# Performance work log

Hardware: AMD Instinct MI355X
Metric: run time of the kernel (lower is better)

Reference implementation:

```python
import jax, jax.numpy as jnp
import numpy as np

KERNEL = 4  # conv kernel == stride (non-overlapping patches)


def _conv(x, W, b):
    # x: [B, Cin, H, W], W: [Cout, Cin, k, k] (OIHW), stride == kernel, VALID padding
    y = jax.lax.conv_general_dilated(
        x, W, window_strides=(KERNEL, KERNEL), padding='VALID',
        dimension_numbers=('NCHW', 'OIHW', 'NCHW'))
    return y + b[None, :, None, None]


def setup_inputs() -> dict:
    key = jax.random.key(0)
    ks = jax.random.split(key, 7)
    B, Cin, H, Wd = 4, 64, 256, 256
    Cout = 128
    s = 0.05
    return {
        'x': jax.random.normal(ks[0], (B, Cin, H, Wd), dtype=jnp.float32),
        'Wq': jax.random.normal(ks[1], (Cout, Cin, KERNEL, KERNEL), dtype=jnp.float32) * s,
        'bq': jax.random.normal(ks[2], (Cout,), dtype=jnp.float32) * s,
        'Wk': jax.random.normal(ks[3], (Cout, Cin, KERNEL, KERNEL), dtype=jnp.float32) * s,
        'bk': jax.random.normal(ks[4], (Cout,), dtype=jnp.float32) * s,
        'Wv': jax.random.normal(ks[5], (Cout, Cin, KERNEL, KERNEL), dtype=jnp.float32) * s,
        'bv': jax.random.normal(ks[6], (Cout,), dtype=jnp.float32) * s,
    }


def reference(x, Wq, bq, Wk, bk, Wv, bv):
    B = x.shape[0]
    q = _conv(x, Wq, bq)              # [B, O, Hp, Wp]
    O, Hp, Wp = q.shape[1], q.shape[2], q.shape[3]
    N = Hp * Wp
    q = q.reshape(B, O, N)
    k = _conv(x, Wk, bk).reshape(B, O, N)
    v = _conv(x, Wv, bv).reshape(B, O, N)
    # scores[b, n, m] = sum_o q[b,o,n] * k[b,o,m]  (NO scaling, as in original)
    scores = jnp.einsum('bon,bom->bnm', q, k)
    attn = jax.nn.softmax(scores, axis=-1)        # [B, N, N]
    # attended^T: out[b, o, n] = sum_m attn[b,n,m] * v[b,o,m]
    out = jnp.einsum('bnm,bom->bon', attn, v)
    return out.reshape(B, O, Hp, Wp)
```

## Files before the change

### kernel.cpp

```cpp
#include <hip/hip_runtime.h>
#include <cstdint>
#include <cstddef>

#define NB 4
#define NP 4096
#define OD 128

typedef _Float16 h16;
typedef _Float16 h16x8 __attribute__((ext_vector_type(8)));
typedef _Float16 h16x4 __attribute__((ext_vector_type(4)));
typedef float    f32x4 __attribute__((ext_vector_type(4)));

__device__ __forceinline__ void async16(const void* g, void* l) {
    __builtin_amdgcn_global_load_lds(
        (const __attribute__((address_space(1))) void*)g,
        (__attribute__((address_space(3))) void*)l, 16, 0, 0);
}

__global__ __launch_bounds__(256) void wcvt(
    const float* __restrict__ Wq, const float* __restrict__ Wk,
    const float* __restrict__ Wv, h16* __restrict__ W16s)
{
    int g = blockIdx.x * 256 + threadIdx.x;
    int mat = g >> 14, r = g & 16383;
    int kc = r >> 9, q = r & 511, o = q >> 2, csw = q & 3;
    int c = csw ^ ((o >> 1) & 3);
    const float* W = (mat == 0) ? Wq : (mat == 1) ? Wk : Wv;
    const float* src = W + (size_t)o * 1024 + kc * 32 + 8 * c;
    f32x4 a = *(const f32x4*)src;
    f32x4 b = *(const f32x4*)(src + 4);
    h16x8 h = {(h16)a.x, (h16)a.y, (h16)a.z, (h16)a.w,
               (h16)b.x, (h16)b.y, (h16)b.z, (h16)b.w};
    *(h16x8*)&W16s[(size_t)g * 8] = h;
}

__global__ __launch_bounds__(256, 2) void conv_qkv(
    const float* __restrict__ x, const h16* __restrict__ W16s,
    const float* __restrict__ bq, const float* __restrict__ bk,
    const float* __restrict__ bv,
    h16* __restrict__ qt, h16* __restrict__ kt, h16* __restrict__ vt)
{
    const int nt = blockIdx.x;
    const int b  = blockIdx.y;
    const int tid = threadIdx.x, lane = tid & 63, wv = tid >> 6;
    const int lr = lane & 15, qd = lane >> 4;
    const int o_w = 32 * wv;

    __shared__ __align__(16) char smem[85504];
    float* biasl = (float*)(smem + 83968);
    if (tid < 128) {
        biasl[tid] = bq[tid]; biasl[128 + tid] = bk[tid]; biasl[256 + tid] = bv[tid];
    }

    auto dmaW = [&](int kc, int bs) {
#pragma unroll
        for (int t = 0; t < 6; ++t) {
            int grp = wv * 6 + t;
            int mat = grp >> 3, sg = grp & 7;
            async16(W16s + ((size_t)(mat * 32 + kc) * 512 + sg * 64 + lane) * 8,
                    smem + bs * 24576 + mat * 8192 + sg * 1024);
        }
    };

    f32x4 xr[2][2];
    auto xload = [&](int kc, int sl) {
        int n = tid >> 2, kg = tid & 3;
        int c = kg >> 1, kh2 = (kg & 1) * 2;
        const float* p = &x[(((size_t)(b * 64 + 2 * kc + c) * 256) + 4 * nt + kh2) * 256 + 4 * n];
        xr[sl][0] = *(const f32x4*)p;
        xr[sl][1] = *(const f32x4*)(p + 256);
    };
    auto xwrite = [&](int sl, int xbs) {
        int n = tid >> 2, kg = tid & 3;
        int c = kg >> 1, kh2 = (kg & 1) * 2;
        h16x8 h = {(h16)xr[sl][0].x, (h16)xr[sl][0].y, (h16)xr[sl][0].z, (h16)xr[sl][0].w,
                   (h16)xr[sl][1].x, (h16)xr[sl][1].y, (h16)xr[sl][1].z, (h16)xr[sl][1].w};
        *(h16x8*)(smem + 73728 + xbs * 5120 + n * 80 + c * 32 + kh2 * 8) = h;
    };

    f32x4 acc[3][2][4];
#pragma unroll
    for (int m = 0; m < 3; ++m)
#pragma unroll
        for (int a = 0; a < 2; ++a)
#pragma unroll
            for (int c = 0; c < 4; ++c) acc[m][a][c] = (f32x4){0.f, 0.f, 0.f, 0.f};

    xload(0, 0); dmaW(0, 0);
    xload(1, 1); dmaW(1, 1);
    xwrite(0, 0);
    __syncthreads();

    int wb = 0;
#pragma unroll 2
    for (int kc = 0; kc < 32; ++kc) {
        int xbs = kc & 1;
        if (kc + 2 < 32) {
            dmaW(kc + 2, (wb == 0) ? 2 : wb - 1);
            xload(kc + 2, xbs);
        }
        const h16* Xl = (const h16*)(smem + 73728 + xbs * 5120);
        const char* Wl = smem + wb * 24576;

        h16x8 bf[4];
#pragma unroll
        for (int tn = 0; tn < 4; ++tn)
            bf[tn] = *(const h16x8*)&Xl[(16 * tn + lr) * 40 + 8 * qd];
#pragma unroll
        for (int mat = 0; mat < 3; ++mat) {
            h16x8 af[2];
#pragma unroll
            for (int to = 0; to < 2; ++to) {
                int o = o_w + 16 * to + lr;
                af[to] = *(const h16x8*)(Wl + mat * 8192 + (size_t)(o * 4 + (qd ^ ((o >> 1) & 3))) * 16);
            }
#pragma unroll
            for (int to = 0; to < 2; ++to)
#pragma unroll
                for (int tn = 0; tn < 4; ++tn)
                    acc[mat][to][tn] = __builtin_amdgcn_mfma_f32_16x16x32_f16(af[to], bf[tn], acc[mat][to][tn], 0, 0, 0);
        }
        if (kc + 1 < 32) xwrite((kc + 1) & 1, 1 - xbs);
        wb = (wb == 2) ? 0 : wb + 1;
        __syncthreads();
    }

    const int n0 = nt * 64;
#pragma unroll
    for (int mat = 0; mat < 2; ++mat) {
        h16* bnc = (h16*)smem;
#pragma unroll
        for (int to = 0; to < 2; ++to)
#pragma unroll
            for (int tn = 0; tn < 4; ++tn) {
                int ob = o_w + 16 * to + 4 * qd;
                int n  = 16 * tn + lr;
                h16x4 hv = {(h16)(acc[mat][to][tn][0] + biasl[mat * 128 + ob]),
                            (h16)(acc[mat][to][tn][1] + biasl[mat * 128 + ob + 1]),
                            (h16)(acc[mat][to][tn][2] + biasl[mat * 128 + ob + 2]),
                            (h16)(acc[mat][to][tn][3] + biasl[mat * 128 + ob + 3])};
                *(h16x4*)&bnc[n * 136 + ob] = hv;
            }
        __syncthreads();
        h16* dst = mat ? kt : qt;
#pragma unroll
        for (int j = 0; j < 4; ++j) {
            int s = tid + 256 * j;
            int n = s >> 4, oc = s & 15;
            *(h16x8*)(dst + ((size_t)(b * NP + n0 + n)) * OD + 8 * oc) = *(h16x8*)&bnc[n * 136 + 8 * oc];
        }
        __syncthreads();
    }
    {
        h16* bnc = (h16*)smem;
#pragma unroll
        for (int to = 0; to < 2; ++to)
#pragma unroll
            for (int tn = 0; tn < 4; ++tn)
#pragma unroll
                for (int r = 0; r < 4; ++r) {
                    int o = o_w + 16 * to + 4 * qd + r;
                    int n = 16 * tn + lr;
                    bnc[o * 72 + n] = (h16)(acc[2][to][tn][r] + biasl[256 + o]);
                }
        __syncthreads();
#pragma unroll
        for (int j = 0; j < 4; ++j) {
            int s = tid + 256 * j;
            int o = s >> 3, ch = s & 7;
            int g = ch >> 2, q2 = ch & 3;
            h16x8 hv;
#pragma unroll
            for (int r2 = 0; r2 < 8; ++r2) {
                int mt = r2 >> 2, r = r2 & 3;
                hv[r2] = bnc[o * 72 + 32 * g + 16 * mt + 4 * q2 + r];
            }
            *(h16x8*)(vt + ((size_t)(b * OD + o)) * NP + n0 + 32 * g + 8 * q2) = hv;
        }
    }
}

template <int SP>
__global__ __launch_bounds__(256, 3) void flash_attn(
    const h16* __restrict__ qt, const h16* __restrict__ kt,
    const h16* __restrict__ vt, h16* __restrict__ po, float2* __restrict__ ml)
{
    constexpr int MR  = NP / SP;
    constexpr int NIT = MR / 32;
    const int nt = blockIdx.x, sp = blockIdx.y, b = blockIdx.z;
    const int tid = threadIdx.x, lane = tid & 63, wv = tid >> 6;
    const int lr = lane & 15, qd = lane >> 4;

    __shared__ __align__(16) char smem[32768];

    h16x8 qf[2][4];
#pragma unroll
    for (int rt = 0; rt < 2; ++rt)
#pragma unroll
        for (int kc = 0; kc < 4; ++kc)
            qf[rt][kc] = *(const h16x8*)&qt[((size_t)(b * NP + nt * 128 + 32 * wv + 16 * rt + lr)) * OD
                                            + 32 * kc + 8 * qd];

    float m_run[2] = {-1e30f, -1e30f}, l_run[2] = {0.f, 0.f};
    f32x4 oacc[2][8];
#pragma unroll
    for (int rt = 0; rt < 2; ++rt)
#pragma unroll
        for (int t = 0; t < 8; ++t) oacc[rt][t] = (f32x4){0.f, 0.f, 0.f, 0.f};

    auto dma = [&](int it, int bs) {
        int m0 = sp * MR + it * 32;
#pragma unroll
        for (int t = 0; t < 2; ++t) {
            int s = wv * 128 + t * 64 + lane;
            int m = s >> 4, cst = s & 15, csrc = cst ^ (m & 15);
            async16(kt + ((size_t)(b * NP + m0 + m)) * OD + 8 * csrc,
                    smem + bs * 8192 + (wv * 128 + t * 64) * 16);
        }
#pragma unroll
        for (int t = 0; t < 2; ++t) {
            int s = wv * 128 + t * 64 + lane;
            int o = s >> 2, cst = s & 3, csrc = cst ^ ((o >> 1) & 3);
            async16(vt + ((size_t)(b * OD + o)) * NP + m0 + 8 * csrc,
                    smem + 16384 + bs * 8192 + (wv * 128 + t * 64) * 16);
        }
    };

    dma(0, 0);
    __syncthreads();

#pragma unroll 2
    for (int it = 0; it < NIT; ++it) {
        int c = it & 1;
        if (it + 1 < NIT) dma(it + 1, 1 - c);
        const h16* Kb = (const h16*)(smem + c * 8192);
        const h16* Vb = (const h16*)(smem + 16384 + c * 8192);

        f32x4 sc[2][2];
#pragma unroll
        for (int rt = 0; rt < 2; ++rt)
#pragma unroll
            for (int mt = 0; mt < 2; ++mt) sc[rt][mt] = (f32x4){0.f, 0.f, 0.f, 0.f};
#pragma unroll
        for (int mt = 0; mt < 2; ++mt)
#pragma unroll
            for (int kc = 0; kc < 4; ++kc) {
                h16x8 kf = *(const h16x8*)&Kb[(size_t)((16 * mt + lr) * 16 + ((4 * kc + qd) ^ lr)) * 8];
                sc[0][mt] = __builtin_amdgcn_mfma_f32_16x16x32_f16(kf, qf[0][kc], sc[0][mt], 0, 0, 0);
                sc[1][mt] = __builtin_amdgcn_mfma_f32_16x16x32_f16(kf, qf[1][kc], sc[1][mt], 0, 0, 0);
            }

        h16x4 pf[2][2];
        float al[2];
#pragma unroll
        for (int rt = 0; rt < 2; ++rt) {
            float mx = fmaxf(fmaxf(fmaxf(sc[rt][0][0], sc[rt][0][1]), fmaxf(sc[rt][0][2], sc[rt][0][3])),
                             fmaxf(fmaxf(sc[rt][1][0], sc[rt][1][1]), fmaxf(sc[rt][1][2], sc[rt][1][3])));
            mx = fmaxf(mx, __shfl_xor(mx, 16));
            mx = fmaxf(mx, __shfl_xor(mx, 32));
            float mn = fmaxf(m_run[rt], mx);
            al[rt] = __expf(m_run[rt] - mn);
            m_run[rt] = mn;
            float rs = 0.f;
#pragma unroll
            for (int mt = 0; mt < 2; ++mt)
#pragma unroll
                for (int r = 0; r < 4; ++r) {
                    float e = __expf(sc[rt][mt][r] - mn);
                    sc[rt][mt][r] = e;
                    rs += e;
                }
            rs += __shfl_xor(rs, 16);
            rs += __shfl_xor(rs, 32);
            l_run[rt] = l_run[rt] * al[rt] + rs;
            pf[rt][0] = (h16x4){(h16)sc[rt][0][0], (h16)sc[rt][0][1], (h16)sc[rt][0][2], (h16)sc[rt][0][3]};
            pf[rt][1] = (h16x4){(h16)sc[rt][1][0], (h16)sc[rt][1][1], (h16)sc[rt][1][2], (h16)sc[rt][1][3]};
        }
#pragma unroll
        for (int rt = 0; rt < 2; ++rt)
#pragma unroll
            for (int to = 0; to < 8; ++to)
#pragma unroll
                for (int r = 0; r < 4; ++r) oacc[rt][to][r] *= al[rt];

#pragma unroll
        for (int to = 0; to < 8; ++to) {
            int o = 16 * to + lr;
            h16x8 vv = *(const h16x8*)&Vb[(size_t)(o * 4 + (qd ^ ((o >> 1) & 3))) * 8];
            h16x4 va = __builtin_shufflevector(vv, vv, 0, 1, 2, 3);
            h16x4 vb2 = __builtin_shufflevector(vv, vv, 4, 5, 6, 7);
#pragma unroll
            for (int rt = 0; rt < 2; ++rt) {
                oacc[rt][to] = __builtin_amdgcn_mfma_f32_16x16x16f16(va,  pf[rt][0], oacc[rt][to], 0, 0, 0);
                oacc[rt][to] = __builtin_amdgcn_mfma_f32_16x16x16f16(vb2, pf[rt][1], oacc[rt][to], 0, 0, 0);
            }
        }
        __syncthreads();
    }

    const size_t nbase = (size_t)(sp * NB + b) * NP + nt * 128 + 32 * wv;
    if (qd == 0) {
#pragma unroll
        for (int rt = 0; rt < 2; ++rt)
            ml[nbase + 16 * rt + lr] = make_float2(m_run[rt], l_run[rt]);
    }
    float inv[2] = {1.f / l_run[0], 1.f / l_run[1]};
#pragma unroll
    for (int rt = 0; rt < 2; ++rt)
#pragma unroll
        for (int to = 0; to < 8; ++to) {
            h16x4 hv = {(h16)(oacc[rt][to][0] * inv[rt]), (h16)(oacc[rt][to][1] * inv[rt]),
                        (h16)(oacc[rt][to][2] * inv[rt]), (h16)(oacc[rt][to][3] * inv[rt])};
            *(h16x4*)&po[(nbase + 16 * rt + lr) * OD + 16 * to + 4 * qd] = hv;
        }
}

template <int SP>
__global__ __launch_bounds__(256) void combine(
    const h16* __restrict__ po, const float2* __restrict__ ml,
    float* __restrict__ out)
{
    const int nt = blockIdx.x, b = blockIdx.y;
    const int n0 = nt * 64, tid = threadIdx.x;
    __shared__ float w[SP][64];
    __shared__ float bn[64 * 130];

    if (tid < 64) {
        int n = n0 + tid;
        float m[SP], l[SP], M = -1e30f;
#pragma unroll
        for (int s = 0; s < SP; ++s) {
            float2 v = ml[(size_t)(s * NB + b) * NP + n];
            m[s] = v.x; l[s] = v.y;
            M = fmaxf(M, m[s]);
        }
        float d = 0.f, e[SP];
#pragma unroll
        for (int s = 0; s < SP; ++s) { e[s] = l[s] * __expf(m[s] - M); d += e[s]; }
        float id = 1.f / d;
#pragma unroll
        for (int s = 0; s < SP; ++s) w[s][tid] = e[s] * id;
    }
    __syncthreads();

#pragma unroll
    for (int j = 0; j < 4; ++j) {
        int s = tid + 256 * j;
        int n = s >> 4, oc = s & 15;
        float acc[8];
#pragma unroll
        for (int k = 0; k < 8; ++k) acc[k] = 0.f;
#pragma unroll
        for (int sp = 0; sp < SP; ++sp) {
            h16x8 v = *(const h16x8*)&po[((size_t)(sp * NB + b) * NP + n0 + n) * OD + 8 * oc];
            float ww = w[sp][n];
#pragma unroll
            for (int k = 0; k < 8; ++k) acc[k] += ww * (float)v[k];
        }
#pragma unroll
        for (int k = 0; k < 8; ++k) bn[n * 130 + 8 * oc + k] = acc[k];
    }
    __syncthreads();

#pragma unroll
    for (int j = 0; j < 8; ++j) {
        int s = tid + 256 * j;
        int o = s >> 4, n4 = s & 15;
        f32x4 r = {bn[(4 * n4 + 0) * 130 + o], bn[(4 * n4 + 1) * 130 + o],
                   bn[(4 * n4 + 2) * 130 + o], bn[(4 * n4 + 3) * 130 + o]};
        *(f32x4*)&out[((size_t)(b * OD + o)) * NP + n0 + 4 * n4] = r;
    }
}

extern "C" void kernel_launch(void* const* d_in, const int* in_sizes, int n_in,
                              void* d_out, int out_size, void* d_ws, size_t ws_size,
                              hipStream_t stream) {
    const float* x  = (const float*)d_in[0];
    const float* Wq = (const float*)d_in[1];
    const float* bq = (const float*)d_in[2];
    const float* Wk = (const float*)d_in[3];
    const float* bk = (const float*)d_in[4];
    const float* Wv = (const float*)d_in[5];
    const float* bv = (const float*)d_in[6];

    h16* qtp  = (h16*)d_ws;
    h16* ktp  = qtp + (size_t)NB * NP * OD;
    h16* vtp  = ktp + (size_t)NB * NP * OD;
    h16* W16s = vtp + (size_t)NB * NP * OD;
    h16* po   = W16s + (size_t)3 * 32 * 512 * 8;
    float* out = (float*)d_out;

    wcvt<<<dim3(192), 256, 0, stream>>>(Wq, Wk, Wv, W16s);
    conv_qkv<<<dim3(64, NB), 256, 0, stream>>>(x, W16s, bq, bk, bv, qtp, ktp, vtp);

    const size_t base = 13369344;
    const size_t need8 = base + (size_t)8 * NB * NP * OD * 2 + (size_t)8 * NB * NP * 8;
    if (ws_size >= need8) {
        float2* ml = (float2*)(po + (size_t)8 * NB * NP * OD);
        flash_attn<8><<<dim3(32, 8, NB), 256, 0, stream>>>(qtp, ktp, vtp, po, ml);
        combine<8><<<dim3(64, NB), 256, 0, stream>>>(po, ml, out);
    } else {
        float2* ml = (float2*)(po + (size_t)4 * NB * NP * OD);
        flash_attn<4><<<dim3(32, 4, NB), 256, 0, stream>>>(qtp, ktp, vtp, po, ml);
        combine<4><<<dim3(64, NB), 256, 0, stream>>>(po, ml, out);
    }
}
```

Before: 205.4 us.

## Fold log2e into Q, lazy softmax rescale, and use 16x16x32 PV MFMA

Pre-scales Q and its bias by log2(e) in the conv kernel so the attention softmax can use native exp2 instead of __expf. The running max is updated only when a tile's max exceeds the old one by more than a threshold, which skips most O-accumulator rescaling. The PV product uses one 16x16x32 MFMA in place of two 16x16x16 ones, with packed RTZ fp16 conversion. It also adds s_setprio around the MFMA blocks and advances precomputed DMA pointers. The lazy rescale lets unnormalized exponentials grow up to 2^12 before rescaling, which reduces fp16 headroom in P.

```diff
diff --git a/kernel.cpp b/kernel.cpp
--- a/kernel.cpp
+++ b/kernel.cpp
@@ -9,7 +9,16 @@
 typedef _Float16 h16;
 typedef _Float16 h16x8 __attribute__((ext_vector_type(8)));
 typedef _Float16 h16x4 __attribute__((ext_vector_type(4)));
+typedef _Float16 h16x2 __attribute__((ext_vector_type(2)));
 typedef float    f32x4 __attribute__((ext_vector_type(4)));
+
+#define LOG2E 1.44269504f
+#define RTH   12.0f
+
+__device__ __forceinline__ float fexp2(float x) { return __builtin_amdgcn_exp2f(x); }
+__device__ __forceinline__ h16x2 cvt_pk(float a, float b) {
+    return __builtin_bit_cast(h16x2, __builtin_amdgcn_cvt_pkrtz(a, b));
+}
 
 __device__ __forceinline__ void async16(const void* g, void* l) {
     __builtin_amdgcn_global_load_lds(
@@ -49,7 +58,8 @@
     __shared__ __align__(16) char smem[85504];
     float* biasl = (float*)(smem + 83968);
     if (tid < 128) {
-        biasl[tid] = bq[tid]; biasl[128 + tid] = bk[tid]; biasl[256 + tid] = bv[tid];
+        biasl[tid] = bq[tid] * LOG2E;
+        biasl[128 + tid] = bk[tid]; biasl[256 + tid] = bv[tid];
     }
 
     auto dmaW = [&](int kc, int bs) {
@@ -128,6 +138,7 @@
     const int n0 = nt * 64;
 #pragma unroll
     for (int mat = 0; mat < 2; ++mat) {
+        const float qs = (mat == 0) ? LOG2E : 1.0f;
         h16* bnc = (h16*)smem;
 #pragma unroll
         for (int to = 0; to < 2; ++to)
@@ -135,10 +146,10 @@
             for (int tn = 0; tn < 4; ++tn) {
                 int ob = o_w + 16 * to + 4 * qd;
                 int n  = 16 * tn + lr;
-                h16x4 hv = {(h16)(acc[mat][to][tn][0] + biasl[mat * 128 + ob]),
-                            (h16)(acc[mat][to][tn][1] + biasl[mat * 128 + ob + 1]),
-                            (h16)(acc[mat][to][tn][2] + biasl[mat * 128 + ob + 2]),
-                            (h16)(acc[mat][to][tn][3] + biasl[mat * 128 + ob + 3])};
+                h16x4 hv = {(h16)(acc[mat][to][tn][0] * qs + biasl[mat * 128 + ob]),
+                            (h16)(acc[mat][to][tn][1] * qs + biasl[mat * 128 + ob + 1]),
+                            (h16)(acc[mat][to][tn][2] * qs + biasl[mat * 128 + ob + 2]),
+                            (h16)(acc[mat][to][tn][3] * qs + biasl[mat * 128 + ob + 3])};
                 *(h16x4*)&bnc[n * 136 + ob] = hv;
             }
         __syncthreads();
@@ -208,31 +219,37 @@
 #pragma unroll
         for (int t = 0; t < 8; ++t) oacc[rt][t] = (f32x4){0.f, 0.f, 0.f, 0.f};
 
-    auto dma = [&](int it, int bs) {
-        int m0 = sp * MR + it * 32;
+    const h16* kp[2]; const h16* vp[2];
+#pragma unroll
+    for (int t = 0; t < 2; ++t) {
+        int s = wv * 128 + t * 64 + lane;
+        int m = s >> 4, ck = s & 15;
+        kp[t] = kt + ((size_t)(b * NP + sp * MR + m)) * OD + 8 * (ck ^ (m & 15));
+        int o = s >> 2, cv = s & 3;
+        vp[t] = vt + ((size_t)(b * OD + o)) * NP + sp * MR + 8 * (cv ^ ((o >> 1) & 3));
+    }
+    const int ldw = wv * 2048;
+
+    auto dma = [&](int bs) {
 #pragma unroll
         for (int t = 0; t < 2; ++t) {
-            int s = wv * 128 + t * 64 + lane;
-            int m = s >> 4, cst = s & 15, csrc = cst ^ (m & 15);
-            async16(kt + ((size_t)(b * NP + m0 + m)) * OD + 8 * csrc,
-                    smem + bs * 8192 + (wv * 128 + t * 64) * 16);
+            async16(kp[t], smem + bs * 8192 + ldw + t * 1024);
+            kp[t] += 32 * OD;
         }
 #pragma unroll
         for (int t = 0; t < 2; ++t) {
-            int s = wv * 128 + t * 64 + lane;
-            int o = s >> 2, cst = s & 3, csrc = cst ^ ((o >> 1) & 3);
-            async16(vt + ((size_t)(b * OD + o)) * NP + m0 + 8 * csrc,
-                    smem + 16384 + bs * 8192 + (wv * 128 + t * 64) * 16);
+            async16(vp[t], smem + 16384 + bs * 8192 + ldw + t * 1024);
+            vp[t] += 32;
         }
     };
 
-    dma(0, 0);
+    dma(0);
     __syncthreads();
 
 #pragma unroll 2
     for (int it = 0; it < NIT; ++it) {
         int c = it & 1;
-        if (it + 1 < NIT) dma(it + 1, 1 - c);
+        if (it + 1 < NIT) dma(1 - c);
         const h16* Kb = (const h16*)(smem + c * 8192);
         const h16* Vb = (const h16*)(smem + 16384 + c * 8192);
 
@@ -241,6 +258,7 @@
         for (int rt = 0; rt < 2; ++rt)
 #pragma unroll
             for (int mt = 0; mt < 2; ++mt) sc[rt][mt] = (f32x4){0.f, 0.f, 0.f, 0.f};
+        __builtin_amdgcn_s_setprio(1);
 #pragma unroll
         for (int mt = 0; mt < 2; ++mt)
 #pragma unroll
@@ -249,52 +267,62 @@
                 sc[0][mt] = __builtin_amdgcn_mfma_f32_16x16x32_f16(kf, qf[0][kc], sc[0][mt], 0, 0, 0);
                 sc[1][mt] = __builtin_amdgcn_mfma_f32_16x16x32_f16(kf, qf[1][kc], sc[1][mt], 0, 0, 0);
             }
-
-        h16x4 pf[2][2];
-        float al[2];
+        __builtin_amdgcn_s_setprio(0);
+
+        float mxv[2];
 #pragma unroll
         for (int rt = 0; rt < 2; ++rt) {
             float mx = fmaxf(fmaxf(fmaxf(sc[rt][0][0], sc[rt][0][1]), fmaxf(sc[rt][0][2], sc[rt][0][3])),
                              fmaxf(fmaxf(sc[rt][1][0], sc[rt][1][1]), fmaxf(sc[rt][1][2], sc[rt][1][3])));
             mx = fmaxf(mx, __shfl_xor(mx, 16));
-            mx = fmaxf(mx, __shfl_xor(mx, 32));
-            float mn = fmaxf(m_run[rt], mx);
-            al[rt] = __expf(m_run[rt] - mn);
-            m_run[rt] = mn;
+            mxv[rt] = fmaxf(mx, __shfl_xor(mx, 32));
+        }
+        if (!__all((mxv[0] <= m_run[0] + RTH) & (mxv[1] <= m_run[1] + RTH))) {
+#pragma unroll
+            for (int rt = 0; rt < 2; ++rt) {
+                float mn = fmaxf(m_run[rt], mxv[rt]);
+                float al = fexp2(m_run[rt] - mn);
+                m_run[rt] = mn;
+                l_run[rt] *= al;
+#pragma unroll
+                for (int to = 0; to < 8; ++to)
+#pragma unroll
+                    for (int r = 0; r < 4; ++r) oacc[rt][to][r] *= al;
+            }
+        }
+
+        h16x8 pf8[2];
+#pragma unroll
+        for (int rt = 0; rt < 2; ++rt) {
             float rs = 0.f;
+            h16x2 pw[4];
 #pragma unroll
             for (int mt = 0; mt < 2; ++mt)
 #pragma unroll
-                for (int r = 0; r < 4; ++r) {
-                    float e = __expf(sc[rt][mt][r] - mn);
-                    sc[rt][mt][r] = e;
-                    rs += e;
+                for (int rp = 0; rp < 2; ++rp) {
+                    float e0 = fexp2(sc[rt][mt][2 * rp]     - m_run[rt]);
+                    float e1 = fexp2(sc[rt][mt][2 * rp + 1] - m_run[rt]);
+                    rs += e0 + e1;
+                    pw[2 * mt + rp] = cvt_pk(e0, e1);
                 }
             rs += __shfl_xor(rs, 16);
             rs += __shfl_xor(rs, 32);
-            l_run[rt] = l_run[rt] * al[rt] + rs;
-            pf[rt][0] = (h16x4){(h16)sc[rt][0][0], (h16)sc[rt][0][1], (h16)sc[rt][0][2], (h16)sc[rt][0][3]};
-            pf[rt][1] = (h16x4){(h16)sc[rt][1][0], (h16)sc[rt][1][1], (h16)sc[rt][1][2], (h16)sc[rt][1][3]};
-        }
-#pragma unroll
-        for (int rt = 0; rt < 2; ++rt)
-#pragma unroll
-            for (int to = 0; to < 8; ++to)
-#pragma unroll
-                for (int r = 0; r < 4; ++r) oacc[rt][to][r] *= al[rt];
-
+            l_run[rt] += rs;
+            pf8[rt] = (h16x8){pw[0][0], pw[0][1], pw[1][0], pw[1][1],
+                              pw[2][0], pw[2][1], pw[3][0], pw[3][1]};
+        }
+
+        __builtin_amdgcn_s_setprio(1);
 #pragma unroll
         for (int to = 0; to < 8; ++to) {
             int o = 16 * to + lr;
             h16x8 vv = *(const h16x8*)&Vb[(size_t)(o * 4 + (qd ^ ((o >> 1) & 3))) * 8];
-            h16x4 va = __builtin_shufflevector(vv, vv, 0, 1, 2, 3);
-            h16x4 vb2 = __builtin_shufflevector(vv, vv, 4, 5, 6, 7);
-#pragma unroll
-            for (int rt = 0; rt < 2; ++rt) {
-                oacc[rt][to] = __builtin_amdgcn_mfma_f32_16x16x16f16(va,  pf[rt][0], oacc[rt][to], 0, 0, 0);
-                oacc[rt][to] = __builtin_amdgcn_mfma_f32_16x16x16f16(vb2, pf[rt][1], oacc[rt][to], 0, 0, 0);
-            }
-        }
+#pragma unroll
+            for (int rt = 0; rt < 2; ++rt)
+                oacc[rt][to] = __builtin_amdgcn_mfma_f32_16x16x32_f16(vv, pf8[rt], oacc[rt][to], 0, 0, 0);
+        }
+        __builtin_amdgcn_s_setprio(0);
+
         __syncthreads();
     }
 
@@ -336,7 +364,7 @@
         }
         float d = 0.f, e[SP];
 #pragma unroll
-        for (int s = 0; s < SP; ++s) { e[s] = l[s] * __expf(m[s] - M); d += e[s]; }
+        for (int s = 0; s < SP; ++s) { e[s] = l[s] * fexp2(m[s] - M); d += e[s]; }
         float id = 1.f / d;
 #pragma unroll
         for (int s = 0; s < SP; ++s) w[s][tid] = e[s] * id;
```

After: 191.1 us. 1.07x faster.
